# Optimization experiments

Measured on AMD Instinct MI355X. Metric: run time of the kernel, lower is better.

The kernel has to match this reference:

```python
import jax, jax.numpy as jnp
import numpy as np

EMBED = 768
HEADS = 8
HEAD_DIM = EMBED // HEADS  # 96


def setup_inputs() -> dict:
    key = jax.random.key(0)
    k1, k2, k3, k4, k5 = jax.random.split(key, 5)
    b, n = 4, 2048
    x = jax.random.normal(k1, (b, n, EMBED), dtype=jnp.float32)
    s = 1.0 / np.sqrt(EMBED)
    W_qkv = jax.random.normal(k2, (EMBED, 3 * EMBED), dtype=jnp.float32) * s
    b_qkv = jax.random.normal(k3, (3 * EMBED,), dtype=jnp.float32) * 0.02
    W_proj = jax.random.normal(k4, (EMBED, EMBED), dtype=jnp.float32) * s
    b_proj = jax.random.normal(k5, (EMBED,), dtype=jnp.float32) * 0.02
    return {"x": x, "W_qkv": W_qkv, "b_qkv": b_qkv, "W_proj": W_proj, "b_proj": b_proj}


def reference(x, W_qkv, b_qkv, W_proj, b_proj):
    b, n, _ = x.shape
    qkv = x @ W_qkv + b_qkv  # [b, n, 3*EMBED]
    # rearrange 'b n (h d qkv) -> qkv b h n d': qkv is fastest-varying axis
    qkv = qkv.reshape(b, n, HEADS, HEAD_DIM, 3)
    q = jnp.transpose(qkv[..., 0], (0, 2, 1, 3))  # [b, h, n, d]
    k = jnp.transpose(qkv[..., 1], (0, 2, 1, 3))
    v = jnp.transpose(qkv[..., 2], (0, 2, 1, 3))
    scale = 1.0 / np.sqrt(HEAD_DIM)
    energy = jnp.einsum('bhqd,bhkd->bhqk', q, k) * scale
    attn = jax.nn.softmax(energy, axis=-1)  # dropout p=0 -> identity
    out = jnp.einsum('bhqk,bhkd->bhqd', attn, v)
    out = jnp.transpose(out, (0, 2, 1, 3)).reshape(b, n, EMBED)
    out = out @ W_proj + b_proj
    return out
```

## Files before the change

### kernel.cpp

```cpp
#include <hip/hip_runtime.h>
#include <hip/hip_bf16.h>

#define EMBED 768
#define NHEADS 8
#define HDIM 96
#define SEQ 2048
#define BATCH 4
#define NTOK (BATCH*SEQ)
#define QKVN (3*EMBED)

#define QSCALE 0.14724444f

typedef __attribute__((ext_vector_type(4))) float f32x4;
typedef __attribute__((ext_vector_type(8))) __bf16 bf16x8;

__device__ __forceinline__ unsigned short f2bf(float f) {
  union { float f; unsigned int u; } c; c.f = f;
  unsigned int u = c.u;
  return (unsigned short)((u + 0x7FFFu + ((u >> 16) & 1u)) >> 16);
}

__device__ __forceinline__ unsigned int cvt_pk_bf16(float lo, float hi) {
  unsigned int r;
  asm("v_cvt_pk_bf16_f32 %0, %1, %2" : "=v"(r) : "v"(lo), "v"(hi));
  return r;
}

__device__ __forceinline__ void gload_lds16(const void* g, void* l) {
  __builtin_amdgcn_global_load_lds(
      (const __attribute__((address_space(1))) unsigned int*)g,
      (__attribute__((address_space(3))) unsigned int*)l, 16, 0, 0);
}

__global__ __launch_bounds__(256) void cast_x_kernel(const float4* __restrict__ in,
                                                     ushort4* __restrict__ out, int n4) {
  int i = blockIdx.x * 256 + threadIdx.x;
  if (i >= n4) return;
  float4 v = in[i];
  out[i] = make_ushort4(f2bf(v.x), f2bf(v.y), f2bf(v.z), f2bf(v.w));
}

__global__ __launch_bounds__(256) void transpose_cast_kernel(const float* __restrict__ in,
                                                             unsigned short* __restrict__ out,
                                                             int R, int C, int remap) {
  __shared__ float t[32][33];
  int c0 = blockIdx.x * 32, r0 = blockIdx.y * 32;
  int tx = threadIdx.x & 31, ty = threadIdx.x >> 5;
  #pragma unroll
  for (int i = 0; i < 32; i += 8)
    t[ty + i][tx] = in[(size_t)(r0 + ty + i) * C + c0 + tx];
  __syncthreads();
  #pragma unroll
  for (int i = 0; i < 32; i += 8) {
    int c = c0 + ty + i;
    int rp = remap ? (c % 3) * 768 + c / 3 : c;
    out[(size_t)rp * R + r0 + tx] = f2bf(t[tx][ty + i]);
  }
}

template <int MODE>
__global__ __launch_bounds__(256, 2) void gemm8_kernel(
    const unsigned short* __restrict__ A, const unsigned short* __restrict__ B,
    const float* __restrict__ bias, int K, int NB,
    unsigned short* __restrict__ Qo, unsigned short* __restrict__ Ko,
    unsigned short* __restrict__ Vt, float* __restrict__ out) {
  __shared__ unsigned short As[2][128 * 64];
  __shared__ unsigned short Bs[2][128 * 64];
  const int tid = threadIdx.x;
  const int lane = tid & 63, wid = tid >> 6;
  const int wr = wid >> 1, wc = wid & 1;
  const int l15 = lane & 15, l16 = lane >> 4;
  const int cpx = gridDim.x >> 3;
  const int bid = blockIdx.x;
  const int swz = (bid & 7) * cpx + (bid >> 3);
  const int my = swz / NB, nx = swz - my * NB;
  const int m0 = my * 128, n0 = nx * 128;

  auto stage_half = [&](int buf, int kt, int half) {
    const unsigned short* src = half ? B : A;
    const int base0 = half ? n0 : m0;
    char* dst = (char*)(half ? &Bs[buf][0] : &As[buf][0]);
    #pragma unroll
    for (int i = 0; i < 4; i++) {
      int c = i * 256 + tid;
      int r = c >> 3, s = c & 7;
      gload_lds16(src + (size_t)(base0 + r) * K + kt * 64 + ((s ^ (r & 7)) << 3),
                  dst + (i * 256 + wid * 64) * 16);
    }
  };

  f32x4 acc[4][4] = {};
  const int xr = (l15 & 7) << 4;

  stage_half(0, 0, 0);
  stage_half(0, 0, 1);
  asm volatile("s_waitcnt vmcnt(0)" ::: "memory");
  __builtin_amdgcn_s_barrier();

  const int NT = K >> 6;
  for (int t = 0; t < NT; ++t) {
    const int cur = t & 1;
    const char* Ac = (const char*)&As[cur][0];
    const char* Bc = (const char*)&Bs[cur][0];
    #pragma unroll
    for (int kh = 0; kh < 2; ++kh) {
      bf16x8 af[4], bfr[4];
      #pragma unroll
      for (int mi = 0; mi < 4; mi++)
        af[mi] = *(const bf16x8*)(Ac + (wr * 64 + mi * 16 + l15) * 128 +
                                  ((kh * 64 + l16 * 16) ^ xr));
      #pragma unroll
      for (int ni = 0; ni < 4; ni++)
        bfr[ni] = *(const bf16x8*)(Bc + (wc * 64 + ni * 16 + l15) * 128 +
                                   ((kh * 64 + l16 * 16) ^ xr));
      if (t + 1 < NT) stage_half(cur ^ 1, t + 1, kh);
      __builtin_amdgcn_s_barrier();
      __builtin_amdgcn_s_setprio(1);
      #pragma unroll
      for (int mi = 0; mi < 4; mi++)
        #pragma unroll
        for (int ni = 0; ni < 4; ni++)
          acc[mi][ni] = __builtin_amdgcn_mfma_f32_16x16x32_bf16(af[mi], bfr[ni], acc[mi][ni], 0, 0, 0);
      __builtin_amdgcn_s_setprio(0);
      __builtin_amdgcn_s_barrier();
    }
    asm volatile("s_waitcnt lgkmcnt(0)" ::: "memory");
    asm volatile("s_waitcnt vmcnt(0)" ::: "memory");
    __builtin_amdgcn_sched_barrier(0);
    __builtin_amdgcn_s_barrier();
  }

  if (MODE == 0) {
    #pragma unroll
    for (int mi = 0; mi < 4; mi++) {
      #pragma unroll
      for (int ni = 0; ni < 4; ni++) {
        int base = n0 + wc * 64 + ni * 16;
        int which = base / 768;
        int hd = base - which * 768;
        int h = hd / 96;
        int d0 = hd - h * 96;
        float bb = bias[(hd + l15) * 3 + which];
        int rowb = m0 + wr * 64 + mi * 16 + l16 * 4;
        int bi = rowb >> 11, nnb = rowb & 2047;
        size_t bh = (size_t)(bi * NHEADS + h);
        if (which == 2) {
          int nn2 = (nnb & ~63) | (nnb & 32) | ((nnb & 12) << 1) | ((nnb & 16) >> 2) | (nnb & 3);
          float v0 = acc[mi][ni][0] + bb, v1 = acc[mi][ni][1] + bb;
          float v2 = acc[mi][ni][2] + bb, v3 = acc[mi][ni][3] + bb;
          uint2 pk;
          pk.x = cvt_pk_bf16(v0, v1);
          pk.y = cvt_pk_bf16(v2, v3);
          *(uint2*)(Vt + (bh * HDIM + d0 + l15) * SEQ + nn2) = pk;
        } else {
          #pragma unroll
          for (int j = 0; j < 4; j++) {
            float v = acc[mi][ni][j] + bb;
            int nn = nnb + j;
            if (which == 0) Qo[(bh * SEQ + nn) * HDIM + d0 + l15] = f2bf(v * QSCALE);
            else            Ko[(bh * SEQ + nn) * HDIM + d0 + l15] = f2bf(v);
          }
        }
      }
    }
  } else {
    #pragma unroll
    for (int mi = 0; mi < 4; mi++) {
      #pragma unroll
      for (int ni = 0; ni < 4; ni++) {
        int col = n0 + wc * 64 + ni * 16 + l15;
        float bb = bias[col];
        #pragma unroll
        for (int j = 0; j < 4; j++) {
          int row = m0 + wr * 64 + mi * 16 + l16 * 4 + j;
          out[(size_t)row * EMBED + col] = acc[mi][ni][j] + bb;
        }
      }
    }
  }
}

__global__ __launch_bounds__(256) void attn_kernel(
    const unsigned short* __restrict__ Q, const unsigned short* __restrict__ Kd,
    const unsigned short* __restrict__ Vt, unsigned short* __restrict__ Oa) {
  __shared__ unsigned short Ks[2][64 * 96];
  __shared__ unsigned short Vs[2][96 * 64];

  const int tid = threadIdx.x, lane = tid & 63, wid = tid >> 6;
  const int l15 = lane & 15, l16 = lane >> 4;
  const int bid = blockIdx.x;
  const int swz = (bid & 7) * 64 + (bid >> 3);
  const int qb_ = swz & 15, bh = swz >> 4;
  const int bi = bh >> 3, h = bh & 7;
  const int q0 = qb_ * 128;

  const unsigned short* Qg = Q + ((size_t)bh * SEQ + q0) * HDIM;
  const unsigned short* Kg = Kd + (size_t)bh * SEQ * HDIM;
  const unsigned short* Vg = Vt + (size_t)bh * HDIM * SEQ;

  bf16x8 qf[2][3];
  #pragma unroll
  for (int qb = 0; qb < 2; qb++)
    #pragma unroll
    for (int ks = 0; ks < 3; ks++)
      qf[qb][ks] = *(const bf16x8*)(Qg + (size_t)(wid * 32 + qb * 16 + l15) * HDIM + ks * 32 + l16 * 8);

  auto stageKV = [&](int buf, int k0) {
    #pragma unroll
    for (int i = 0; i < 3; i++) {
      int idx = i * 256 + tid;
      gload_lds16(Kg + (size_t)k0 * HDIM + idx * 8,
                  (char*)&Ks[buf][0] + (i * 256 + wid * 64) * 16);
    }
    #pragma unroll
    for (int i = 0; i < 3; i++) {
      int idx = i * 256 + tid;
      int d = idx >> 3, s = idx & 7;
      gload_lds16(Vg + (size_t)d * SEQ + k0 + ((s ^ (d & 7)) << 3),
                  (char*)&Vs[buf][0] + (i * 256 + wid * 64) * 16);
    }
  };

  f32x4 oacc[2][6] = {};
  float mrow[2], lrow[2];
  mrow[0] = mrow[1] = -__builtin_inff();
  lrow[0] = lrow[1] = 0.f;

  stageKV(0, 0);
  __syncthreads();

  for (int kb = 0; kb < SEQ / 64; kb++) {
    const int cur = kb & 1;
    if (kb + 1 < SEQ / 64) stageKV(cur ^ 1, (kb + 1) * 64);

    const char* Kc = (const char*)&Ks[cur][0];
    const char* Vc = (const char*)&Vs[cur][0];

    f32x4 sacc[2][4] = {};
    #pragma unroll
    for (int ks = 0; ks < 3; ks++) {
      bf16x8 ak[4];
      #pragma unroll
      for (int ni = 0; ni < 4; ni++)
        ak[ni] = *(const bf16x8*)(Kc + (ni * 16 + l15) * 192 + ks * 64 + l16 * 16);
      #pragma unroll
      for (int qb = 0; qb < 2; qb++)
        #pragma unroll
        for (int ni = 0; ni < 4; ni++)
          sacc[qb][ni] = __builtin_amdgcn_mfma_f32_16x16x32_bf16(ak[ni], qf[qb][ks], sacc[qb][ni], 0, 0, 0);
    }

    float tmax[2];
    float g = -3.4e38f;
    #pragma unroll
    for (int qb = 0; qb < 2; qb++) {
      float a0 = fmaxf(fmaxf(sacc[qb][0][0], sacc[qb][0][1]), fmaxf(sacc[qb][0][2], sacc[qb][0][3]));
      float a1 = fmaxf(fmaxf(sacc[qb][1][0], sacc[qb][1][1]), fmaxf(sacc[qb][1][2], sacc[qb][1][3]));
      float a2 = fmaxf(fmaxf(sacc[qb][2][0], sacc[qb][2][1]), fmaxf(sacc[qb][2][2], sacc[qb][2][3]));
      float a3 = fmaxf(fmaxf(sacc[qb][3][0], sacc[qb][3][1]), fmaxf(sacc[qb][3][2], sacc[qb][3][3]));
      float v = fmaxf(fmaxf(a0, a1), fmaxf(a2, a3));
      v = fmaxf(v, __shfl_xor(v, 16));
      v = fmaxf(v, __shfl_xor(v, 32));
      tmax[qb] = v;
      g = fmaxf(g, v - mrow[qb]);
    }
    if (!__all(g <= 11.54f)) {
      #pragma unroll
      for (int qb = 0; qb < 2; qb++) {
        float mnew = fmaxf(mrow[qb], tmax[qb]);
        float alpha = __builtin_amdgcn_exp2f(mrow[qb] - mnew);
        mrow[qb] = mnew;
        lrow[qb] *= alpha;
        #pragma unroll
        for (int d6 = 0; d6 < 6; d6++) {
          oacc[qb][d6][0] *= alpha; oacc[qb][d6][1] *= alpha;
          oacc[qb][d6][2] *= alpha; oacc[qb][d6][3] *= alpha;
        }
      }
    }

    unsigned int pk[2][8];
    #pragma unroll
    for (int qb = 0; qb < 2; qb++) {
      const float m = mrow[qb];
      float psum = 0.f;
      #pragma unroll
      for (int ni = 0; ni < 4; ni++) {
        float p0 = __builtin_amdgcn_exp2f(sacc[qb][ni][0] - m);
        float p1 = __builtin_amdgcn_exp2f(sacc[qb][ni][1] - m);
        float p2 = __builtin_amdgcn_exp2f(sacc[qb][ni][2] - m);
        float p3 = __builtin_amdgcn_exp2f(sacc[qb][ni][3] - m);
        psum += (p0 + p1) + (p2 + p3);
        pk[qb][ni * 2]     = cvt_pk_bf16(p0, p1);
        pk[qb][ni * 2 + 1] = cvt_pk_bf16(p2, p3);
      }
      psum += __shfl_xor(psum, 16);
      psum += __shfl_xor(psum, 32);
      lrow[qb] += psum;
    }

    #pragma unroll
    for (int ks = 0; ks < 2; ks++) {
      bf16x8 vb[6];
      #pragma unroll
      for (int d6 = 0; d6 < 6; d6++)
        vb[d6] = *(const bf16x8*)(Vc + (d6 * 16 + l15) * 128 +
                                  (((ks * 4 + l16) ^ (l15 & 7)) << 4));
      #pragma unroll
      for (int qb = 0; qb < 2; qb++) {
        union { unsigned int u[4]; bf16x8 v; } pf;
        pf.u[0] = pk[qb][4 * ks];     pf.u[1] = pk[qb][4 * ks + 1];
        pf.u[2] = pk[qb][4 * ks + 2]; pf.u[3] = pk[qb][4 * ks + 3];
        #pragma unroll
        for (int d6 = 0; d6 < 6; d6++)
          oacc[qb][d6] = __builtin_amdgcn_mfma_f32_16x16x32_bf16(vb[d6], pf.v, oacc[qb][d6], 0, 0, 0);
      }
    }

    __syncthreads();
  }

  #pragma unroll
  for (int qb = 0; qb < 2; qb++) {
    const float rl = 1.f / lrow[qb];
    const int tok = q0 + wid * 32 + qb * 16 + l15;
    unsigned short* Og = Oa + ((size_t)bi * SEQ + tok) * EMBED + h * HDIM;
    #pragma unroll
    for (int d6 = 0; d6 < 6; d6++) {
      uint2 o;
      o.x = cvt_pk_bf16(oacc[qb][d6][0] * rl, oacc[qb][d6][1] * rl);
      o.y = cvt_pk_bf16(oacc[qb][d6][2] * rl, oacc[qb][d6][3] * rl);
      *(uint2*)(Og + d6 * 16 + l16 * 4) = o;
    }
  }
}

extern "C" void kernel_launch(void* const* d_in, const int* in_sizes, int n_in,
                              void* d_out, int out_size, void* d_ws, size_t ws_size,
                              hipStream_t stream) {
  const float* x      = (const float*)d_in[0];
  const float* W_qkv  = (const float*)d_in[1];
  const float* b_qkv  = (const float*)d_in[2];
  const float* W_proj = (const float*)d_in[3];
  const float* b_proj = (const float*)d_in[4];
  float* out = (float*)d_out;

  char* ws = (char*)d_ws;
  size_t off = 0;
  auto alloc = [&](size_t bytes) { void* p = ws + off; off += (bytes + 255) & ~(size_t)255; return p; };
  unsigned short* xb  = (unsigned short*)alloc((size_t)NTOK * EMBED * 2);
  unsigned short* WqT = (unsigned short*)alloc((size_t)QKVN * EMBED * 2);
  unsigned short* WpT = (unsigned short*)alloc((size_t)EMBED * EMBED * 2);
  unsigned short* Qb  = (unsigned short*)alloc((size_t)NTOK * EMBED * 2);
  unsigned short* Kb  = (unsigned short*)alloc((size_t)NTOK * EMBED * 2);
  unsigned short* Vtb = (unsigned short*)alloc((size_t)NTOK * EMBED * 2);
  unsigned short* Ob  = (unsigned short*)alloc((size_t)NTOK * EMBED * 2);

  cast_x_kernel<<<dim3(NTOK * EMBED / 4 / 256), dim3(256), 0, stream>>>(
      (const float4*)x, (ushort4*)xb, NTOK * EMBED / 4);
  transpose_cast_kernel<<<dim3(QKVN / 32, EMBED / 32), dim3(256), 0, stream>>>(W_qkv, WqT, EMBED, QKVN, 1);
  transpose_cast_kernel<<<dim3(EMBED / 32, EMBED / 32), dim3(256), 0, stream>>>(W_proj, WpT, EMBED, EMBED, 0);

  gemm8_kernel<0><<<dim3((NTOK / 128) * (QKVN / 128)), dim3(256), 0, stream>>>(
      xb, WqT, b_qkv, EMBED, QKVN / 128, Qb, Kb, Vtb, nullptr);

  attn_kernel<<<dim3(BATCH * NHEADS * (SEQ / 128)), dim3(256), 0, stream>>>(Qb, Kb, Vtb, Ob);

  gemm8_kernel<1><<<dim3((NTOK / 128) * (EMBED / 128)), dim3(256), 0, stream>>>(
      Ob, WpT, b_proj, EMBED, EMBED / 128, nullptr, nullptr, nullptr, out);
}
```

Baseline: 157.6 us.

## Use eight waves per attention block with one 16-row query tile each

Result: no change. 159.2 us (+1.0%).

```diff
diff --git a/kernel.cpp b/kernel.cpp
--- a/kernel.cpp
+++ b/kernel.cpp
@@ -180,7 +180,7 @@
   }
 }
 
-__global__ __launch_bounds__(256) void attn_kernel(
+__global__ __launch_bounds__(512) void attn_kernel(
     const unsigned short* __restrict__ Q, const unsigned short* __restrict__ Kd,
     const unsigned short* __restrict__ Vt, unsigned short* __restrict__ Oa) {
   __shared__ unsigned short Ks[2][64 * 96];
@@ -198,33 +198,30 @@
   const unsigned short* Kg = Kd + (size_t)bh * SEQ * HDIM;
   const unsigned short* Vg = Vt + (size_t)bh * HDIM * SEQ;
 
-  bf16x8 qf[2][3];
+  bf16x8 qf[3];
   #pragma unroll
-  for (int qb = 0; qb < 2; qb++)
-    #pragma unroll
-    for (int ks = 0; ks < 3; ks++)
-      qf[qb][ks] = *(const bf16x8*)(Qg + (size_t)(wid * 32 + qb * 16 + l15) * HDIM + ks * 32 + l16 * 8);
+  for (int ks = 0; ks < 3; ks++)
+    qf[ks] = *(const bf16x8*)(Qg + (size_t)(wid * 16 + l15) * HDIM + ks * 32 + l16 * 8);
 
   auto stageKV = [&](int buf, int k0) {
-    #pragma unroll
-    for (int i = 0; i < 3; i++) {
-      int idx = i * 256 + tid;
-      gload_lds16(Kg + (size_t)k0 * HDIM + idx * 8,
-                  (char*)&Ks[buf][0] + (i * 256 + wid * 64) * 16);
-    }
-    #pragma unroll
-    for (int i = 0; i < 3; i++) {
-      int idx = i * 256 + tid;
-      int d = idx >> 3, s = idx & 7;
+    gload_lds16(Kg + (size_t)k0 * HDIM + tid * 8, (char*)&Ks[buf][0] + wid * 1024);
+    if (wid < 4)
+      gload_lds16(Kg + (size_t)k0 * HDIM + (512 + tid) * 8,
+                  (char*)&Ks[buf][0] + 8192 + wid * 1024);
+    {
+      int d = tid >> 3, s = tid & 7;
       gload_lds16(Vg + (size_t)d * SEQ + k0 + ((s ^ (d & 7)) << 3),
-                  (char*)&Vs[buf][0] + (i * 256 + wid * 64) * 16);
+                  (char*)&Vs[buf][0] + wid * 1024);
+    }
+    if (wid < 4) {
+      int idx = 512 + tid, d = idx >> 3, s = idx & 7;
+      gload_lds16(Vg + (size_t)d * SEQ + k0 + ((s ^ (d & 7)) << 3),
+                  (char*)&Vs[buf][0] + 8192 + wid * 1024);
     }
   };
 
-  f32x4 oacc[2][6] = {};
-  float mrow[2], lrow[2];
-  mrow[0] = mrow[1] = -__builtin_inff();
-  lrow[0] = lrow[1] = 0.f;
+  f32x4 oacc[6] = {};
+  float mrow = -__builtin_inff(), lrow = 0.f;
 
   stageKV(0, 0);
   __syncthreads();
@@ -236,67 +233,55 @@
     const char* Kc = (const char*)&Ks[cur][0];
     const char* Vc = (const char*)&Vs[cur][0];
 
-    f32x4 sacc[2][4] = {};
+    f32x4 sacc[4] = {};
     #pragma unroll
     for (int ks = 0; ks < 3; ks++) {
       bf16x8 ak[4];
       #pragma unroll
       for (int ni = 0; ni < 4; ni++)
         ak[ni] = *(const bf16x8*)(Kc + (ni * 16 + l15) * 192 + ks * 64 + l16 * 16);
-      #pragma unroll
-      for (int qb = 0; qb < 2; qb++)
-        #pragma unroll
-        for (int ni = 0; ni < 4; ni++)
-          sacc[qb][ni] = __builtin_amdgcn_mfma_f32_16x16x32_bf16(ak[ni], qf[qb][ks], sacc[qb][ni], 0, 0, 0);
-    }
-
-    float tmax[2];
-    float g = -3.4e38f;
-    #pragma unroll
-    for (int qb = 0; qb < 2; qb++) {
-      float a0 = fmaxf(fmaxf(sacc[qb][0][0], sacc[qb][0][1]), fmaxf(sacc[qb][0][2], sacc[qb][0][3]));
-      float a1 = fmaxf(fmaxf(sacc[qb][1][0], sacc[qb][1][1]), fmaxf(sacc[qb][1][2], sacc[qb][1][3]));
-      float a2 = fmaxf(fmaxf(sacc[qb][2][0], sacc[qb][2][1]), fmaxf(sacc[qb][2][2], sacc[qb][2][3]));
-      float a3 = fmaxf(fmaxf(sacc[qb][3][0], sacc[qb][3][1]), fmaxf(sacc[qb][3][2], sacc[qb][3][3]));
-      float v = fmaxf(fmaxf(a0, a1), fmaxf(a2, a3));
-      v = fmaxf(v, __shfl_xor(v, 16));
-      v = fmaxf(v, __shfl_xor(v, 32));
-      tmax[qb] = v;
-      g = fmaxf(g, v - mrow[qb]);
-    }
-    if (!__all(g <= 11.54f)) {
-      #pragma unroll
-      for (int qb = 0; qb < 2; qb++) {
-        float mnew = fmaxf(mrow[qb], tmax[qb]);
-        float alpha = __builtin_amdgcn_exp2f(mrow[qb] - mnew);
-        mrow[qb] = mnew;
-        lrow[qb] *= alpha;
-        #pragma unroll
-        for (int d6 = 0; d6 < 6; d6++) {
-          oacc[qb][d6][0] *= alpha; oacc[qb][d6][1] *= alpha;
-          oacc[qb][d6][2] *= alpha; oacc[qb][d6][3] *= alpha;
-        }
+      __builtin_amdgcn_s_setprio(1);
+      #pragma unroll
+      for (int ni = 0; ni < 4; ni++)
+        sacc[ni] = __builtin_amdgcn_mfma_f32_16x16x32_bf16(ak[ni], qf[ks], sacc[ni], 0, 0, 0);
+      __builtin_amdgcn_s_setprio(0);
+    }
+
+    float a0 = fmaxf(fmaxf(sacc[0][0], sacc[0][1]), fmaxf(sacc[0][2], sacc[0][3]));
+    float a1 = fmaxf(fmaxf(sacc[1][0], sacc[1][1]), fmaxf(sacc[1][2], sacc[1][3]));
+    float a2 = fmaxf(fmaxf(sacc[2][0], sacc[2][1]), fmaxf(sacc[2][2], sacc[2][3]));
+    float a3 = fmaxf(fmaxf(sacc[3][0], sacc[3][1]), fmaxf(sacc[3][2], sacc[3][3]));
+    float v = fmaxf(fmaxf(a0, a1), fmaxf(a2, a3));
+    v = fmaxf(v, __shfl_xor(v, 16));
+    v = fmaxf(v, __shfl_xor(v, 32));
+    if (!__all(v - mrow <= 11.54f)) {
+      float mnew = fmaxf(mrow, v);
+      float alpha = __builtin_amdgcn_exp2f(mrow - mnew);
+      mrow = mnew;
+      lrow *= alpha;
+      #pragma unroll
+      for (int d6 = 0; d6 < 6; d6++) {
+        oacc[d6][0] *= alpha; oacc[d6][1] *= alpha;
+        oacc[d6][2] *= alpha; oacc[d6][3] *= alpha;
       }
     }
 
-    unsigned int pk[2][8];
-    #pragma unroll
-    for (int qb = 0; qb < 2; qb++) {
-      const float m = mrow[qb];
+    unsigned int pk[8];
+    {
       float psum = 0.f;
       #pragma unroll
       for (int ni = 0; ni < 4; ni++) {
-        float p0 = __builtin_amdgcn_exp2f(sacc[qb][ni][0] - m);
-        float p1 = __builtin_amdgcn_exp2f(sacc[qb][ni][1] - m);
-        float p2 = __builtin_amdgcn_exp2f(sacc[qb][ni][2] - m);
-        float p3 = __builtin_amdgcn_exp2f(sacc[qb][ni][3] - m);
+        float p0 = __builtin_amdgcn_exp2f(sacc[ni][0] - mrow);
+        float p1 = __builtin_amdgcn_exp2f(sacc[ni][1] - mrow);
+        float p2 = __builtin_amdgcn_exp2f(sacc[ni][2] - mrow);
+        float p3 = __builtin_amdgcn_exp2f(sacc[ni][3] - mrow);
         psum += (p0 + p1) + (p2 + p3);
-        pk[qb][ni * 2]     = cvt_pk_bf16(p0, p1);
-        pk[qb][ni * 2 + 1] = cvt_pk_bf16(p2, p3);
+        pk[ni * 2]     = cvt_pk_bf16(p0, p1);
+        pk[ni * 2 + 1] = cvt_pk_bf16(p2, p3);
       }
       psum += __shfl_xor(psum, 16);
       psum += __shfl_xor(psum, 32);
-      lrow[qb] += psum;
+      lrow += psum;
     }
 
     #pragma unroll
@@ -306,30 +291,28 @@
       for (int d6 = 0; d6 < 6; d6++)
         vb[d6] = *(const bf16x8*)(Vc + (d6 * 16 + l15) * 128 +
                                   (((ks * 4 + l16) ^ (l15 & 7)) << 4));
-      #pragma unroll
-      for (int qb = 0; qb < 2; qb++) {
-        union { unsigned int u[4]; bf16x8 v; } pf;
-        pf.u[0] = pk[qb][4 * ks];     pf.u[1] = pk[qb][4 * ks + 1];
-        pf.u[2] = pk[qb][4 * ks + 2]; pf.u[3] = pk[qb][4 * ks + 3];
-        #pragma unroll
-        for (int d6 = 0; d6 < 6; d6++)
-          oacc[qb][d6] = __builtin_amdgcn_mfma_f32_16x16x32_bf16(vb[d6], pf.v, oacc[qb][d6], 0, 0, 0);
-      }
+      union { unsigned int u[4]; bf16x8 v; } pf;
+      pf.u[0] = pk[4 * ks];     pf.u[1] = pk[4 * ks + 1];
+      pf.u[2] = pk[4 * ks + 2]; pf.u[3] = pk[4 * ks + 3];
+      __builtin_amdgcn_s_setprio(1);
+      #pragma unroll
+      for (int d6 = 0; d6 < 6; d6++)
+        oacc[d6] = __builtin_amdgcn_mfma_f32_16x16x32_bf16(vb[d6], pf.v, oacc[d6], 0, 0, 0);
+      __builtin_amdgcn_s_setprio(0);
     }
 
     __syncthreads();
   }
 
-  #pragma unroll
-  for (int qb = 0; qb < 2; qb++) {
-    const float rl = 1.f / lrow[qb];
-    const int tok = q0 + wid * 32 + qb * 16 + l15;
+  {
+    const float rl = 1.f / lrow;
+    const int tok = q0 + wid * 16 + l15;
     unsigned short* Og = Oa + ((size_t)bi * SEQ + tok) * EMBED + h * HDIM;
     #pragma unroll
     for (int d6 = 0; d6 < 6; d6++) {
       uint2 o;
-      o.x = cvt_pk_bf16(oacc[qb][d6][0] * rl, oacc[qb][d6][1] * rl);
-      o.y = cvt_pk_bf16(oacc[qb][d6][2] * rl, oacc[qb][d6][3] * rl);
+      o.x = cvt_pk_bf16(oacc[d6][0] * rl, oacc[d6][1] * rl);
+      o.y = cvt_pk_bf16(oacc[d6][2] * rl, oacc[d6][3] * rl);
       *(uint2*)(Og + d6 * 16 + l16 * 4) = o;
     }
   }
@@ -364,7 +347,7 @@
   gemm8_kernel<0><<<dim3((NTOK / 128) * (QKVN / 128)), dim3(256), 0, stream>>>(
       xb, WqT, b_qkv, EMBED, QKVN / 128, Qb, Kb, Vtb, nullptr);
 
-  attn_kernel<<<dim3(BATCH * NHEADS * (SEQ / 128)), dim3(256), 0, stream>>>(Qb, Kb, Vtb, Ob);
+  attn_kernel<<<dim3(BATCH * NHEADS * (SEQ / 128)), dim3(512), 0, stream>>>(Qb, Kb, Vtb, Ob);
 
   gemm8_kernel<1><<<dim3((NTOK / 128) * (EMBED / 128)), dim3(256), 0, stream>>>(
       Ob, WpT, b_proj, EMBED, EMBED / 128, nullptr, nullptr, nullptr, out);
```
